# Kernel tuning notes

Hardware: AMD Instinct MI355X
Metric: run time of the kernel (lower is better)

Reference implementation:

```python
import jax, jax.numpy as jnp
import numpy as np

IN_CHANNELS = 64
OUT_CHANNELS = 64
SEQ_LEN = 512
KERNEL_SIZE = 9
STRIDE = 1
PADDING = 4  # symmetric
OUT_SEQ_LEN = (SEQ_LEN + 2 * PADDING - (KERNEL_SIZE - 1) - 1) // STRIDE + 1  # 512


def setup_inputs() -> dict:
    key = jax.random.key(0)
    k1, k2, k3 = jax.random.split(key, 3)
    x = jax.random.normal(k1, (64, IN_CHANNELS, SEQ_LEN), dtype=jnp.float32)
    # nn.init.normal_(std=0.1)
    weight = 0.1 * jax.random.normal(k2, (IN_CHANNELS, OUT_CHANNELS, KERNEL_SIZE, OUT_SEQ_LEN), dtype=jnp.float32)
    bias = 0.1 * jax.random.normal(k3, (OUT_CHANNELS, OUT_SEQ_LEN), dtype=jnp.float32)
    return {"x": x, "weight": weight, "bias": bias}


def reference(x, weight, bias):
    # x: [B, Ci, S] -> pad last dim
    xp = jnp.pad(x, ((0, 0), (0, 0), (PADDING, PADDING)))
    # Unfold (im2col) as a gather: same math as the one-hot grouped conv.
    starts = jnp.arange(OUT_SEQ_LEN) * STRIDE            # [L]
    offs = jnp.arange(KERNEL_SIZE)                        # [K]
    idx = starts[:, None] + offs[None, :]                 # [L, K]
    patches = xp[:, :, idx]                               # [B, Ci, L, K]
    # per-position matmul: 'b i l k, i o k l -> b o l'
    out = jnp.einsum('bilk,iokl->bol', patches, weight)
    out = out + bias                                      # [B, Co, L]
    return out
```

## Files before the change

### kernel.cpp

```cpp
#include <hip/hip_runtime.h>


#define CIN   64
#define COUT  64
#define SEQ   512
#define KS    9
#define LT    16
#define OT    8
#define LWIN  24
#define WSTR  (COUT*KS*SEQ)
#define XBS   40
#define XLW   (64*XBS)
#define XS_ELEMS (LWIN*XLW)
#define BOS   40
#define BLS   (OT*BOS + 8)
#define BSLOT (LT*BLS)
#define ZOFF  (XS_ELEMS + 2*BSLOT)
#define LDS_USH (ZOFF + 64)
#define LDS_BYTES (LDS_USH*2)
#define NSTEP 18

typedef __attribute__((ext_vector_type(8))) short bf16x8;
typedef __attribute__((ext_vector_type(4))) float f32x4;

__device__ __forceinline__ uint pack2bf(float a0, float a1) {
    uint u0 = __float_as_uint(a0) + 0x8000u;
    uint u1 = __float_as_uint(a1) + 0x8000u;
    return __builtin_amdgcn_perm(u1, u0, 0x07060302);
}

__global__ __launch_bounds__(1024, 4)
void lc1d_mfma(const float* __restrict__ x, const float* __restrict__ w,
               const float* __restrict__ bias, float* __restrict__ out)
{
    extern __shared__ ushort lds[];
    ushort* Xs = lds;
    ushort* BsB = lds + XS_ELEMS;

    const int tid  = threadIdx.x;
    const int lane = tid & 63;
    const int wvid = tid >> 6;
    const int bt = wvid & 3;
    const int lg = wvid >> 2;
    const int lt = blockIdx.x >> 3;
    const int os = blockIdx.x & 7;
    const int l0 = lt * LT;
    const int o0 = os * OT;

    const bool stager = (tid < 512);
    const int lf  = tid & 3;
    const int oo  = (tid >> 2) & 7;
    const int ipp = (tid >> 5) & 15;

    const float* wbase = w + ((size_t)(2*ipp)*COUT + (o0 + oo))*(KS*SEQ) + l0 + lf*4;

    float4 rA[3], rB[3];

    #define LOAD_RING(sl, s) if (stager && (s) < NSTEP) {                        \
        const int ih_ = (s) / 9, k_ = (s) - 9*ih_;                               \
        const float* p_ = wbase + (size_t)ih_*32*WSTR + k_*SEQ;                  \
        rA[sl] = *(const float4*)p_;                                             \
        rB[sl] = *(const float4*)(p_ + WSTR);                                    \
    }

    #define WRITE_BS(sl, s) if (stager) {                                        \
        ushort* dst_ = BsB + ((s)&1)*BSLOT + oo*BOS + 2*ipp;                     \
        _Pragma("unroll")                                                        \
        for (int dl = 0; dl < 4; ++dl) {                                         \
            uint pk_ = pack2bf((&rA[sl].x)[dl], (&rB[sl].x)[dl]);                \
            *(uint*)(dst_ + (lf*4+dl)*BLS) = pk_;                                \
        }                                                                        \
    }

    #define STAGE_XS(ih) {                                                       \
        const int qq  = tid & 7;                                                 \
        const int rp0 = tid >> 3;                                                \
        if (qq < 6) {                                                            \
            _Pragma("unroll")                                                    \
            for (int it = 0; it < 8; ++it) {                                     \
                const int rp = rp0 + it*128;                                     \
                const int b_ = rp >> 4, ip_ = rp & 15;                           \
                const float* s0 = x + ((size_t)(b_*CIN) + (ih)*32 + 2*ip_)*SEQ   \
                                    + (l0 - 4) + qq*4;                           \
                float4 v0 = make_float4(0.f,0.f,0.f,0.f), v1 = v0;               \
                if (!((lt == 0 && qq == 0) || (lt == 31 && qq == 5))) {          \
                    v0 = *(const float4*)s0;                                     \
                    v1 = *(const float4*)(s0 + SEQ);                             \
                }                                                                \
                ushort* d_ = Xs + b_*XBS + 2*ip_;                                \
                _Pragma("unroll")                                                \
                for (int dl = 0; dl < 4; ++dl)                                   \
                    *(uint*)(d_ + (qq*4+dl)*XLW) = pack2bf((&v0.x)[dl],          \
                                                           (&v1.x)[dl]);         \
            }                                                                    \
        }                                                                        \
    }

    const int aoff = (bt*16 + (lane & 15))*XBS + (lane >> 4)*8;
    const int boff = (lane & 15)*BOS + (lane >> 4)*8;
    const bool nhi = (lane & 15) >= 8;
    const ushort* zptr = lds + ZOFF + (lane >> 4)*8;

    f32x4 acc[4];
    #pragma unroll
    for (int j = 0; j < 4; ++j) acc[j] = (f32x4)0.0f;

    #define DO_MFMA(s) {                                                         \
        const int k_ = (s) % 9;                                                  \
        const ushort* BsS = BsB + ((s)&1)*BSLOT;                                 \
        _Pragma("unroll")                                                        \
        for (int dl = 0; dl < 4; ++dl) {                                         \
            const int ll = lg*4 + dl;                                            \
            bf16x8 Af = *(const bf16x8*)(Xs + (ll + k_)*XLW + aoff);             \
            const ushort* Bp = nhi ? zptr : (BsS + ll*BLS + boff);               \
            bf16x8 Bf = *(const bf16x8*)Bp;                                      \
            acc[dl] = __builtin_amdgcn_mfma_f32_16x16x32_bf16(Af, Bf, acc[dl],   \
                                                              0, 0, 0);          \
        }                                                                        \
    }

    #define STEP(s) {                                                            \
        if ((s) < NSTEP-1) WRITE_BS(((s)+1)%3, (s)+1)                            \
        LOAD_RING(((s)+1)%3, (s)+4)                                              \
        DO_MFMA(s)                                                               \
        __syncthreads();                                                         \
    }

    LOAD_RING(0, 0)
    LOAD_RING(1, 1)
    LOAD_RING(2, 2)
    if (tid < 64) lds[ZOFF + tid] = 0;
    STAGE_XS(0)
    WRITE_BS(0, 0)
    LOAD_RING(0, 3)
    __syncthreads();

    STEP(0)  STEP(1)  STEP(2)  STEP(3)  STEP(4)
    STEP(5)  STEP(6)  STEP(7)  STEP(8)

    STAGE_XS(1)
    __syncthreads();

    STEP(9)  STEP(10) STEP(11) STEP(12) STEP(13)
    STEP(14) STEP(15) STEP(16) STEP(17)

    if (!nhi) {
        const int og = o0 + (lane & 15);
        const int rb = (lane >> 4)*4;
        #pragma unroll
        for (int dl = 0; dl < 4; ++dl) {
            const int lgl = l0 + lg*4 + dl;
            const float bv = bias[og*SEQ + lgl];
            #pragma unroll
            for (int r = 0; r < 4; ++r) {
                const int bg = bt*16 + rb + r;
                out[((size_t)(bg*COUT + og))*SEQ + lgl] = acc[dl][r] + bv;
            }
        }
    }
}

extern "C" void kernel_launch(void* const* d_in, const int* in_sizes, int n_in,
                              void* d_out, int out_size, void* d_ws, size_t ws_size,
                              hipStream_t stream) {
    const float* x    = (const float*)d_in[0];
    const float* wgt  = (const float*)d_in[1];
    const float* bias = (const float*)d_in[2];
    float* out        = (float*)d_out;

    hipFuncSetAttribute((const void*)lc1d_mfma,
                        hipFuncAttributeMaxDynamicSharedMemorySize, LDS_BYTES);
    dim3 grid(256);
    lc1d_mfma<<<grid, 1024, LDS_BYTES, stream>>>(x, wgt, bias, out);
}
```

Before: 133.8 us.

## Prefetch second X slab into registers and use LDS-only barriers

The X staging for the second input-channel half is split into a global-load phase and an LDS-write phase. The loads are issued early, between steps 5 and 6, so their latency overlaps the MFMA steps 6–8. Every __syncthreads is replaced with a barrier that waits only on lgkmcnt, not vmcnt, so the weight ring and X prefetch loads can stay in flight across barriers. The cost is 64 extra VGPRs per thread for the prefetched X values, which under the tight launch bounds may cause spills or lower occupancy.

```diff
diff --git a/kernel.cpp b/kernel.cpp
--- a/kernel.cpp
+++ b/kernel.cpp
@@ -29,6 +29,12 @@
     return __builtin_amdgcn_perm(u1, u0, 0x07060302);
 }
 
+#define BAR() do {                                                           \
+    asm volatile("s_waitcnt lgkmcnt(0)" ::: "memory");                       \
+    __builtin_amdgcn_s_barrier();                                            \
+    asm volatile("" ::: "memory");                                           \
+} while (0)
+
 __global__ __launch_bounds__(1024, 4)
 void lc1d_mfma(const float* __restrict__ x, const float* __restrict__ w,
                const float* __restrict__ bias, float* __restrict__ out)
@@ -55,6 +61,7 @@
     const float* wbase = w + ((size_t)(2*ipp)*COUT + (o0 + oo))*(KS*SEQ) + l0 + lf*4;
 
     float4 rA[3], rB[3];
+    float4 xv0[8], xv1[8];
 
     #define LOAD_RING(sl, s) if (stager && (s) < NSTEP) {                        \
         const int ih_ = (s) / 9, k_ = (s) - 9*ih_;                               \
@@ -72,7 +79,27 @@
         }                                                                        \
     }
 
-    #define STAGE_XS(ih) {                                                       \
+    #define STAGE_XS_LOAD(ih) {                                                  \
+        const int qq  = tid & 7;                                                 \
+        const int rp0 = tid >> 3;                                                \
+        const bool act = (qq < 6) &&                                             \
+                         !((lt == 0 && qq == 0) || (lt == 31 && qq == 5));       \
+        _Pragma("unroll")                                                        \
+        for (int it = 0; it < 8; ++it) {                                         \
+            const int rp = rp0 + it*128;                                         \
+            const int b_ = rp >> 4, ip_ = rp & 15;                               \
+            const float* s0 = x + ((size_t)(b_*CIN) + (ih)*32 + 2*ip_)*SEQ       \
+                                + (l0 - 4) + qq*4;                               \
+            xv0[it] = make_float4(0.f,0.f,0.f,0.f);                              \
+            xv1[it] = xv0[it];                                                   \
+            if (act) {                                                           \
+                xv0[it] = *(const float4*)s0;                                    \
+                xv1[it] = *(const float4*)(s0 + SEQ);                            \
+            }                                                                    \
+        }                                                                        \
+    }
+
+    #define STAGE_XS_WRITE() {                                                   \
         const int qq  = tid & 7;                                                 \
         const int rp0 = tid >> 3;                                                \
         if (qq < 6) {                                                            \
@@ -80,18 +107,11 @@
             for (int it = 0; it < 8; ++it) {                                     \
                 const int rp = rp0 + it*128;                                     \
                 const int b_ = rp >> 4, ip_ = rp & 15;                           \
-                const float* s0 = x + ((size_t)(b_*CIN) + (ih)*32 + 2*ip_)*SEQ   \
-                                    + (l0 - 4) + qq*4;                           \
-                float4 v0 = make_float4(0.f,0.f,0.f,0.f), v1 = v0;               \
-                if (!((lt == 0 && qq == 0) || (lt == 31 && qq == 5))) {          \
-                    v0 = *(const float4*)s0;                                     \
-                    v1 = *(const float4*)(s0 + SEQ);                             \
-                }                                                                \
                 ushort* d_ = Xs + b_*XBS + 2*ip_;                                \
                 _Pragma("unroll")                                                \
                 for (int dl = 0; dl < 4; ++dl)                                   \
-                    *(uint*)(d_ + (qq*4+dl)*XLW) = pack2bf((&v0.x)[dl],          \
-                                                           (&v1.x)[dl]);         \
+                    *(uint*)(d_ + (qq*4+dl)*XLW) =                               \
+                        pack2bf((&xv0[it].x)[dl], (&xv1[it].x)[dl]);             \
             }                                                                    \
         }                                                                        \
     }
@@ -123,23 +143,28 @@
         if ((s) < NSTEP-1) WRITE_BS(((s)+1)%3, (s)+1)                            \
         LOAD_RING(((s)+1)%3, (s)+4)                                              \
         DO_MFMA(s)                                                               \
-        __syncthreads();                                                         \
-    }
-
+        BAR();                                                                   \
+    }
+
+    STAGE_XS_LOAD(0)
     LOAD_RING(0, 0)
     LOAD_RING(1, 1)
     LOAD_RING(2, 2)
     if (tid < 64) lds[ZOFF + tid] = 0;
-    STAGE_XS(0)
+    STAGE_XS_WRITE()
     WRITE_BS(0, 0)
     LOAD_RING(0, 3)
-    __syncthreads();
+    BAR();
 
     STEP(0)  STEP(1)  STEP(2)  STEP(3)  STEP(4)
-    STEP(5)  STEP(6)  STEP(7)  STEP(8)
-
-    STAGE_XS(1)
-    __syncthreads();
+    STEP(5)
+
+    STAGE_XS_LOAD(1)
+
+    STEP(6)  STEP(7)  STEP(8)
+
+    STAGE_XS_WRITE()
+    BAR();
 
     STEP(9)  STEP(10) STEP(11) STEP(12) STEP(13)
     STEP(14) STEP(15) STEP(16) STEP(17)
```

Measured after the change: 148.1 us. 10.7% more time.
